# Optimization experiments

Hardware: AMD Instinct MI355X
Metric: run time of the kernel (lower is better)

Reference implementation:

```python
import jax
import jax.numpy as jnp
import numpy as np
from jax import lax

DELTA = float(np.exp(-2.0))  # rule-creation density threshold


def codebook_lamb(x):
    """Online growing RBF prototype codebook (ALMMo-style) for one layer.

    x: [N, M]. Returns lamb: [N] normalized density of each sample at its
    assigned rule. Faithful (corrected) semantics of Layer.__call__:
      - SEN = squared L2 norm per sample (over feature dim)
      - global mean / mean squared norm over the batch
      - sequential per-sample: if max RBF density over existing rules < exp(-2),
        append a new rule (prototype=c=x, SENc=||x||^2, support=1);
        else update rule_star. Note the source's `support[rule_star] = +1`
        assigns 1, so the running mean update degenerates to c[rule_star]=x,
        SENc[rule_star]=||x||^2 -- replicated here.
      - distances use the (never-updated) prototypes; bandwidth stau uses c.
    """
    N, M = x.shape
    SENx = jnp.sum(x * x, axis=-1)                      # [N]
    gmean = jnp.mean(x, axis=0)                         # [M]
    base = jnp.mean(SENx) - jnp.sum(gmean * gmean)      # SENgmean - SEN(gmean)
    R = N                                               # worst case: one rule/sample

    protos0 = jnp.zeros((R, M), x.dtype)
    pn20 = jnp.zeros((R,), x.dtype)                     # ||proto_r||^2 (carried)
    c0 = jnp.zeros((R, M), x.dtype)
    cn20 = jnp.zeros((R,), x.dtype)                     # ||c_r||^2 (carried)
    SENc0 = jnp.zeros((R,), x.dtype)
    count0 = jnp.int32(0)

    ridx = jnp.arange(R)

    def step(carry, inp):
        protos, pn2, c, cn2, SENc, count = carry
        xi, sxi = inp                                   # [M], scalar
        valid = ridx < count
        stau = (base + SENc - cn2) * 0.5                # [R]
        dist = sxi + pn2 - 2.0 * (protos @ xi)          # [R] ||xi - proto_r||^2
        dens = jnp.where(valid, jnp.exp(-dist / stau), -jnp.inf)
        idx = jnp.argmax(dens)
        vmax = dens[idx]
        new = (count == 0) | (vmax < DELTA)
        slot = jnp.where(new, count, idx)
        # both branches set c/SENc at slot to xi/sxi (support resets to 1)
        c = c.at[slot].set(xi)
        cn2 = cn2.at[slot].set(sxi)
        SENc = SENc.at[slot].set(sxi)
        # only a new rule writes a prototype (OOB scatter when count==R is dropped)
        protos = protos.at[count].set(jnp.where(new, xi, protos[count]))
        pn2 = pn2.at[count].set(jnp.where(new, sxi, pn2[count]))
        count = count + new.astype(count.dtype)
        return (protos, pn2, c, cn2, SENc, count), slot

    (protos, pn2, c, cn2, SENc, count), rules = lax.scan(
        step, (protos0, pn20, c0, cn20, SENc0, count0), (x, SENx)
    )

    # final densities of all samples under all (valid) rules: [R, N]
    stau = (base + SENc - cn2) * 0.5                    # [R]
    dist = SENx[None, :] + pn2[:, None] - 2.0 * (protos @ x.T)
    dens = jnp.where((ridx < count)[:, None], jnp.exp(-dist / stau[:, None]), 0.0)
    dens_xn = dens[rules, jnp.arange(N)]                # density at assigned rule
    lamb = dens_xn / jnp.sum(dens, axis=0)              # normalize over rules
    return lamb


def setup_inputs() -> dict:
    key = jax.random.key(0)
    k = jax.random.split(key, 5)
    N, D_IN, D_H, D_OUT = 2048, 2048, 2048, 1024
    s0 = 1.0 / np.sqrt(D_IN)
    s1 = 1.0 / np.sqrt(D_H)
    return {
        "x": jax.random.normal(k[0], (N, D_IN), jnp.float32),
        "W0": jax.random.normal(k[1], (D_H, D_IN), jnp.float32) * s0,
        "b0": jax.random.normal(k[2], (D_H,), jnp.float32) * s0,
        "W1": jax.random.normal(k[3], (D_OUT, D_H), jnp.float32) * s1,
        "b1": jax.random.normal(k[4], (D_OUT,), jnp.float32) * s1,
    }


def reference(x, W0, b0, W1, b1):
    lambs = []
    h = x
    for W, b in ((W0, b0), (W1, b1)):
        lambs.append(codebook_lamb(h))          # per-layer codebook on layer input
        h = jax.nn.sigmoid(h @ W.T + b)         # torch.nn.Linear + sigmoid
    return h, jnp.stack(lambs)                  # ([N, d_out], [n_layers, N])
```

## Files before the change

### kernel.cpp

```cpp
#include <hip/hip_runtime.h>
#include <cstdint>
#include <cstddef>


#define DELTA_F 0.13533528323661270f
#define MBYTE (1u << 20)

typedef __bf16 bf16;
typedef bf16 bf16x8 __attribute__((ext_vector_type(8)));
typedef bf16 bf16x4 __attribute__((ext_vector_type(4)));
typedef float f32x4 __attribute__((ext_vector_type(4)));

typedef __attribute__((address_space(1))) void as1_void;
typedef __attribute__((address_space(3))) void as3_void;

__device__ __forceinline__ void gload16(const bf16* g, bf16* l) {
  __builtin_amdgcn_global_load_lds((as1_void*)g, (as3_void*)l, 16, 0, 0);
}

template <bool SIG_B16>
__global__ __launch_bounds__(512, 4) void gemm_fused(
    const bf16* __restrict__ A, const bf16* __restrict__ Bm,
    float* __restrict__ G, bf16* __restrict__ Hb, float* __restrict__ Fo,
    const float* __restrict__ bias, float* __restrict__ SEN,
    float* __restrict__ sumAll, int K, int sigW) {
  __shared__ __align__(16) char smem[32768];
  const int tid = threadIdx.x;
  const int wave = tid >> 6, lane = tid & 63;
  const int quad = lane >> 4, l16 = lane & 15;
  const int kg = wave & 1, wm = (wave >> 1) & 1, wn = (wave >> 2) & 1;
  const int m0 = blockIdx.y * 128, n0 = blockIdx.x * 128;
  const int waveM = wm * 64, waveN = wn * 64;
  const bool isGram = (n0 < 2048);
  const int sr8 = lane >> 3, slot = lane & 7;
  const int gk = (slot ^ sr8) * 8;
  const bf16* aSrc = A + (size_t)(m0 + wave * 16 + sr8) * K + gk;
  const bf16* bSrc = Bm + (size_t)(n0 + wave * 16 + sr8) * K + gk;
  char* const aDst = smem + wave * 2048;
  char* const bDst = smem + 16384 + wave * 2048;
  const int swz = ((kg * 4 + quad) ^ (l16 & 7)) * 16;
  const int aOff = (waveM + l16) * 128 + swz;
  const int bOff = 16384 + (waveN + l16) * 128 + swz;

  f32x4 acc[4][4] = {};

  for (int k0 = 0; k0 < K; k0 += 64) {
    gload16(aSrc + k0, (bf16*)aDst);
    gload16(aSrc + 8 * (size_t)K + k0, (bf16*)(aDst + 1024));
    gload16(bSrc + k0, (bf16*)bDst);
    gload16(bSrc + 8 * (size_t)K + k0, (bf16*)(bDst + 1024));
    __syncthreads();
    bf16x8 af[4], bfr[4];
#pragma unroll
    for (int i = 0; i < 4; ++i) af[i] = *(const bf16x8*)(smem + aOff + i * 2048);
#pragma unroll
    for (int j = 0; j < 4; ++j) bfr[j] = *(const bf16x8*)(smem + bOff + j * 2048);
#pragma unroll
    for (int i = 0; i < 4; ++i)
#pragma unroll
      for (int j = 0; j < 4; ++j)
        acc[i][j] = __builtin_amdgcn_mfma_f32_16x16x32_bf16(af[i], bfr[j], acc[i][j], 0, 0, 0);
    __syncthreads();
  }

  float gsum = 0.f;
  char* const ex = smem + (wn * 2 + wm) * 8192;
#pragma unroll
  for (int round = 0; round < 2; ++round) {
    __syncthreads();
    if (kg == 1) {
#pragma unroll
      for (int ii = 0; ii < 2; ++ii)
#pragma unroll
        for (int j = 0; j < 4; ++j)
          *(f32x4*)(ex + (ii * 4 + j) * 1024 + lane * 16) = acc[round * 2 + ii][j];
    }
    __syncthreads();
    if (kg == 0) {
#pragma unroll
      for (int ii = 0; ii < 2; ++ii) {
        const int i = round * 2 + ii;
#pragma unroll
        for (int j = 0; j < 4; ++j) {
          f32x4 v = acc[i][j] + *(const f32x4*)(ex + (ii * 4 + j) * 1024 + lane * 16);
          const int col = n0 + waveN + j * 16 + l16;
          const float bv = isGram ? 0.f : bias[col - 2048];
#pragma unroll
          for (int r = 0; r < 4; ++r) {
            const int row = m0 + waveM + i * 16 + quad * 4 + r;
            if (isGram) {
              const float val = v[r];
              G[(size_t)row * 2048 + col] = val;
              gsum += val;
              if (row == col) SEN[row] = val;
            } else {
              const float hv = 1.0f / (1.0f + expf(-(v[r] + bv)));
              const int c2 = col - 2048;
              if (SIG_B16) Hb[(size_t)row * 2048 + c2] = (bf16)hv;
              else Fo[(size_t)row * sigW + c2] = hv;
            }
          }
        }
      }
    }
  }
  if (isGram && kg == 0) {
    for (int off = 32; off > 0; off >>= 1) gsum += __shfl_down(gsum, off, 64);
    if (lane == 0) atomicAdd(sumAll, gsum);
  }
}

__device__ __forceinline__ float block_reduce_sum(float s, float* ws4) {
  for (int off = 32; off > 0; off >>= 1) s += __shfl_down(s, off, 64);
  const int tid = threadIdx.x;
  if ((tid & 63) == 0) ws4[tid >> 6] = s;
  __syncthreads();
  return ws4[0] + ws4[1] + ws4[2] + ws4[3];
}

__global__ void f2b_all(const float* __restrict__ x, const float* __restrict__ W0,
                        const float* __restrict__ W1, bf16* __restrict__ xb,
                        bf16* __restrict__ wb0, bf16* __restrict__ wb1,
                        float* __restrict__ scal) {
  const int idx = (blockIdx.x * 256 + threadIdx.x) * 4;
  if (blockIdx.x == 0 && threadIdx.x < 16) scal[threadIdx.x] = 0.f;
  const float* src;
  bf16* dst;
  int off;
  if (idx < 4194304) { src = x; dst = xb; off = idx; }
  else if (idx < 8388608) { src = W0; dst = wb0; off = idx - 4194304; }
  else { src = W1; dst = wb1; off = idx - 8388608; }
  f32x4 v = *(const f32x4*)(src + off);
  bf16x4 o;
  o.x = (bf16)v.x; o.y = (bf16)v.y; o.z = (bf16)v.z; o.w = (bf16)v.w;
  *(bf16x4*)(dst + off) = o;
}

__global__ void stau_kernel(const float* __restrict__ SEN, float* __restrict__ base,
                            int Nsamp) {
  const int tid = threadIdx.x;
  float s = 0.f;
  for (int i = tid; i < Nsamp; i += 256) s += SEN[i];
  __shared__ float ws4[4];
  const float tot = block_reduce_sum(s, ws4);
  if (tid == 0) {
    const float invN = 1.0f / (float)Nsamp;
    const float stau = 0.5f * (tot * invN - base[2] * invN * invN);
    base[0] = stau;
    base[1] = -1.0f / stau;
  }
}

__global__ void edgesum_kernel(const float* __restrict__ G, const float* __restrict__ SEN,
                               const float* __restrict__ base, int N,
                               int* __restrict__ e, float* __restrict__ S) {
  const int i = blockIdx.x, tid = threadIdx.x;
  const float ninv = base[1];
  const float si = SEN[i];
  const float* gi = G + (size_t)i * N;
  __shared__ int sflag;
  if (tid == 0) sflag = 0;
  __syncthreads();
  float s = 0.f;
  int f = 0;
  for (int j = tid; j < N; j += 256) {
    const float dens = expf((si + SEN[j] - 2.0f * gi[j]) * ninv);
    s += dens;
    if (j < i && dens >= DELTA_F) f = 1;
  }
  if (f) atomicOr(&sflag, 1);
  __shared__ float ws4[4];
  const float tot = block_reduce_sum(s, ws4);
  __syncthreads();
  if (tid == 0) { e[i] = sflag; S[i] = tot; }
}

__global__ void decide_kernel(const int* __restrict__ e, const float* __restrict__ G,
                              const float* __restrict__ SEN, const float* __restrict__ base,
                              int N, int* __restrict__ newflag, int* __restrict__ assigned,
                              int* __restrict__ rcnt, int* __restrict__ rlist) {
  __shared__ int s_flag[2048];
  __shared__ short s_list[2048];
  __shared__ short s_re[2048];
  __shared__ int s_T, s_reN;
  __shared__ int scan[256];
  __shared__ float rbest[256];
  __shared__ int rbj[256];
  const int tid = threadIdx.x;
  const float ninv = base[1];
  const int per = N / 256;
  int cnt = 0;
  for (int k = 0; k < per; ++k) {
    const int i = tid * per + k;
    const int ei = e[i];
    s_flag[i] = (ei == 0);
    if (ei == 0) { newflag[i] = 1; assigned[i] = i; }
    cnt += ei;
  }
  scan[tid] = cnt;
  if (tid == 0) s_reN = 0;
  __syncthreads();
  for (int off = 1; off < 256; off <<= 1) {
    const int v = scan[tid];
    const int add = (tid >= off) ? scan[tid - off] : 0;
    __syncthreads();
    scan[tid] = v + add;
    __syncthreads();
  }
  int pos = scan[tid] - cnt;
  for (int k = 0; k < per; ++k) {
    const int i = tid * per + k;
    if (!s_flag[i]) s_list[pos++] = (short)i;
  }
  if (tid == 255) s_T = scan[255];
  __syncthreads();
  const int T = s_T;
  for (int t = 0; t < T; ++t) {
    const int i = s_list[t];
    const float si = SEN[i];
    const float* gi = G + (size_t)i * N;
    float best = -1.0f;
    int bestj = 0x7fffffff;
    for (int j = tid; j < i; j += 256) {
      if (s_flag[j]) {
        const float dens = expf((si + SEN[j] - 2.0f * gi[j]) * ninv);
        if (dens > best || (dens == best && j < bestj)) { best = dens; bestj = j; }
      }
    }
    rbest[tid] = best; rbj[tid] = bestj;
    __syncthreads();
    if (tid == 0) {
      float b = -1.0f;
      int bj = 0x7fffffff;
      for (int k = 0; k < 256; ++k)
        if (rbest[k] > b || (rbest[k] == b && rbj[k] < bj)) { b = rbest[k]; bj = rbj[k]; }
      if (b < DELTA_F) { s_flag[i] = 1; newflag[i] = 1; assigned[i] = i; }
      else { newflag[i] = 0; assigned[i] = bj; s_re[s_reN++] = (short)i; }
    }
    __syncthreads();
  }
  const int reN = s_reN;
  for (int t = tid; t < reN; t += 256) rlist[t] = s_re[t];
  if (tid == 0) rcnt[0] = reN;
}

__global__ void lamb_fix(const float* __restrict__ G, const float* __restrict__ SEN,
                         const float* __restrict__ base, const float* __restrict__ S,
                         const int* __restrict__ assigned, const int* __restrict__ rcnt,
                         const int* __restrict__ rlist, int N, float* __restrict__ lamb) {
  const int n = blockIdx.x * 256 + threadIdx.x;
  const float ninv = base[1];
  const float sn = SEN[n];
  const float* gn = G + (size_t)n * N;
  const int a = assigned[n];
  const float da = expf((sn + SEN[a] - 2.0f * gn[a]) * ninv);
  float denom = S[n];
  const int rc = rcnt[0];
  for (int t = 0; t < rc; ++t) {
    const int j = rlist[t];
    denom -= expf((sn + SEN[j] - 2.0f * gn[j]) * ninv);
  }
  lamb[n] = da / denom;
}

extern "C" void kernel_launch(void* const* d_in, const int* in_sizes, int n_in,
                              void* d_out, int out_size, void* d_ws, size_t ws_size,
                              hipStream_t stream) {
  const float* x = (const float*)d_in[0];
  const float* W0 = (const float*)d_in[1];
  const float* b0 = (const float*)d_in[2];
  const float* W1 = (const float*)d_in[3];
  const float* b1 = (const float*)d_in[4];
  float* out = (float*)d_out;

  const int N = 2048, DIN = 2048, DH = 2048, DOUT = 1024;

  char* w = (char*)d_ws;
  bf16* xb = (bf16*)(w);
  bf16* wb0 = (bf16*)(w + 8 * MBYTE);
  bf16* hb = (bf16*)(w + 16 * MBYTE);
  bf16* wb1 = (bf16*)(w + 24 * MBYTE);
  float* G = (float*)(w + 28 * MBYTE);
  float* SEN = (float*)(w + 44 * MBYTE);
  float* S = SEN + 2048;
  float* scal = S + 2048;
  int* e = (int*)(scal + 16);
  int* nf = e + 2048;
  int* as = nf + 2048;
  int* rcnt = as + 2048;
  int* rlist = rcnt + 16;

  float* lamb0 = out + (size_t)N * DOUT;
  float* lamb1 = lamb0 + N;

  f2b_all<<<10240, 256, 0, stream>>>(x, W0, W1, xb, wb0, wb1, scal);

  gemm_fused<true><<<dim3(32, 16), 512, 0, stream>>>(
      xb, xb, G, hb, nullptr, b0, SEN, scal + 2, DIN, DH);
  stau_kernel<<<1, 256, 0, stream>>>(SEN, scal + 0, N);
  edgesum_kernel<<<N, 256, 0, stream>>>(G, SEN, scal + 0, N, e, S);
  decide_kernel<<<1, 256, 0, stream>>>(e, G, SEN, scal + 0, N, nf, as, rcnt, rlist);
  lamb_fix<<<N / 256, 256, 0, stream>>>(G, SEN, scal + 0, S, as, rcnt, rlist, N, lamb0);

  gemm_fused<false><<<dim3(24, 16), 512, 0, stream>>>(
      hb, hb, G, nullptr, out, b1, SEN, scal + 6, DH, DOUT);
  stau_kernel<<<1, 256, 0, stream>>>(SEN, scal + 4, N);
  edgesum_kernel<<<N, 256, 0, stream>>>(G, SEN, scal + 4, N, e, S);
  decide_kernel<<<1, 256, 0, stream>>>(e, G, SEN, scal + 4, N, nf, as, rcnt, rlist);
  lamb_fix<<<N / 256, 256, 0, stream>>>(G, SEN, scal + 4, S, as, rcnt, rlist, N, lamb1);
}
```

Before: 231.6 us.

## Fuse density, row sums and edge flags into GEMM epilogue; precompute stau

The stau bandwidth is now computed before each Gram GEMM: for layer 0 from row norms and column sums produced during the bf16 conversion, and for layer 1 from norms and column sums accumulated in the layer-0 sigmoid epilogue. The GEMM epilogue can therefore write densities directly, accumulate per-row density sums and set the edge flags with atomics. This removes the separate edgesum pass over the Gram matrix and the recomputation of exp in the decide and lamb kernels. The lamb step is folded into the single-block decide kernel, which serializes that work onto one block, and the many extra atomics plus fast __expf bring some throughput and precision risk.

```diff
diff --git a/kernel.cpp b/kernel.cpp
--- a/kernel.cpp
+++ b/kernel.cpp
@@ -18,12 +18,14 @@
   __builtin_amdgcn_global_load_lds((as1_void*)g, (as3_void*)l, 16, 0, 0);
 }
 
-template <bool SIG_B16>
+template <bool IS_L0>
 __global__ __launch_bounds__(512, 4) void gemm_fused(
-    const bf16* __restrict__ A, const bf16* __restrict__ Bm,
-    float* __restrict__ G, bf16* __restrict__ Hb, float* __restrict__ Fo,
-    const float* __restrict__ bias, float* __restrict__ SEN,
-    float* __restrict__ sumAll, int K, int sigW) {
+    const bf16* __restrict__ A, float* __restrict__ Dens,
+    bf16* __restrict__ Hb, float* __restrict__ Fo,
+    const float* __restrict__ bias, const float* __restrict__ SENin,
+    const float* __restrict__ ninv_p, float* __restrict__ S,
+    int* __restrict__ e, float* __restrict__ SENhOut,
+    float* __restrict__ colsumH) {
   __shared__ __align__(16) char smem[32768];
   const int tid = threadIdx.x;
   const int wave = tid >> 6, lane = tid & 63;
@@ -34,8 +36,8 @@
   const bool isGram = (n0 < 2048);
   const int sr8 = lane >> 3, slot = lane & 7;
   const int gk = (slot ^ sr8) * 8;
-  const bf16* aSrc = A + (size_t)(m0 + wave * 16 + sr8) * K + gk;
-  const bf16* bSrc = Bm + (size_t)(n0 + wave * 16 + sr8) * K + gk;
+  const bf16* aSrc = A + (size_t)(m0 + wave * 16 + sr8) * 2048 + gk;
+  const bf16* bSrc = A + (size_t)(n0 + wave * 16 + sr8) * 2048 + gk;
   char* const aDst = smem + wave * 2048;
   char* const bDst = smem + 16384 + wave * 2048;
   const int swz = ((kg * 4 + quad) ^ (l16 & 7)) * 16;
@@ -43,12 +45,11 @@
   const int bOff = 16384 + (waveN + l16) * 128 + swz;
 
   f32x4 acc[4][4] = {};
-
-  for (int k0 = 0; k0 < K; k0 += 64) {
+  for (int k0 = 0; k0 < 2048; k0 += 64) {
     gload16(aSrc + k0, (bf16*)aDst);
-    gload16(aSrc + 8 * (size_t)K + k0, (bf16*)(aDst + 1024));
+    gload16(aSrc + 8 * 2048 + k0, (bf16*)(aDst + 1024));
     gload16(bSrc + k0, (bf16*)bDst);
-    gload16(bSrc + 8 * (size_t)K + k0, (bf16*)(bDst + 1024));
+    gload16(bSrc + 8 * 2048 + k0, (bf16*)(bDst + 1024));
     __syncthreads();
     bf16x8 af[4], bfr[4];
 #pragma unroll
@@ -63,7 +64,8 @@
     __syncthreads();
   }
 
-  float gsum = 0.f;
+  const float ninv = ninv_p[0];
+  float colp[4] = {0.f, 0.f, 0.f, 0.f};
   char* const ex = smem + (wn * 2 + wm) * 8192;
 #pragma unroll
   for (int round = 0; round < 2; ++round) {
@@ -80,151 +82,242 @@
 #pragma unroll
       for (int ii = 0; ii < 2; ++ii) {
         const int i = round * 2 + ii;
-#pragma unroll
-        for (int j = 0; j < 4; ++j) {
-          f32x4 v = acc[i][j] + *(const f32x4*)(ex + (ii * 4 + j) * 1024 + lane * 16);
-          const int col = n0 + waveN + j * 16 + l16;
-          const float bv = isGram ? 0.f : bias[col - 2048];
+        const int rbase = m0 + waveM + i * 16 + quad * 4;
+        if (isGram) {
+          const f32x4 si4 = *(const f32x4*)(SENin + rbase);
+          float rp[4] = {0.f, 0.f, 0.f, 0.f};
+          int er = 0;
+#pragma unroll
+          for (int j = 0; j < 4; ++j) {
+            f32x4 v = acc[i][j] + *(const f32x4*)(ex + (ii * 4 + j) * 1024 + lane * 16);
+            const int col = n0 + waveN + j * 16 + l16;
+            const float sj = SENin[col];
+#pragma unroll
+            for (int r = 0; r < 4; ++r) {
+              const float dens = __expf((si4[r] + sj - 2.0f * v[r]) * ninv);
+              Dens[(size_t)(rbase + r) * 2048 + col] = dens;
+              rp[r] += dens;
+              if (col < rbase + r && dens >= DELTA_F) er |= (1 << r);
+            }
+          }
 #pragma unroll
           for (int r = 0; r < 4; ++r) {
-            const int row = m0 + waveM + i * 16 + quad * 4 + r;
-            if (isGram) {
-              const float val = v[r];
-              G[(size_t)row * 2048 + col] = val;
-              gsum += val;
-              if (row == col) SEN[row] = val;
-            } else {
-              const float hv = 1.0f / (1.0f + expf(-(v[r] + bv)));
-              const int c2 = col - 2048;
-              if (SIG_B16) Hb[(size_t)row * 2048 + c2] = (bf16)hv;
-              else Fo[(size_t)row * sigW + c2] = hv;
+            float rv = rp[r];
+            rv += __shfl_xor(rv, 1, 64); rv += __shfl_xor(rv, 2, 64);
+            rv += __shfl_xor(rv, 4, 64); rv += __shfl_xor(rv, 8, 64);
+            if (l16 == 0) atomicAdd(S + rbase + r, rv);
+          }
+          er |= __shfl_xor(er, 1, 64); er |= __shfl_xor(er, 2, 64);
+          er |= __shfl_xor(er, 4, 64); er |= __shfl_xor(er, 8, 64);
+          if (l16 == 0 && er) {
+#pragma unroll
+            for (int r = 0; r < 4; ++r)
+              if ((er >> r) & 1) atomicOr(e + rbase + r, 1);
+          }
+        } else {
+          float rn[4] = {0.f, 0.f, 0.f, 0.f};
+#pragma unroll
+          for (int j = 0; j < 4; ++j) {
+            f32x4 v = acc[i][j] + *(const f32x4*)(ex + (ii * 4 + j) * 1024 + lane * 16);
+            const int c2 = n0 - 2048 + waveN + j * 16 + l16;
+            const float bv = bias[c2];
+#pragma unroll
+            for (int r = 0; r < 4; ++r) {
+              const float hv = 1.0f / (1.0f + __expf(-(v[r] + bv)));
+              if (IS_L0) {
+                Hb[(size_t)(rbase + r) * 2048 + c2] = (bf16)hv;
+                rn[r] += hv * hv;
+                colp[j] += hv;
+              } else {
+                Fo[(size_t)(rbase + r) * 1024 + c2] = hv;
+              }
+            }
+          }
+          if (IS_L0) {
+#pragma unroll
+            for (int r = 0; r < 4; ++r) {
+              float rv = rn[r];
+              rv += __shfl_xor(rv, 1, 64); rv += __shfl_xor(rv, 2, 64);
+              rv += __shfl_xor(rv, 4, 64); rv += __shfl_xor(rv, 8, 64);
+              if (l16 == 0) atomicAdd(SENhOut + rbase + r, rv);
             }
           }
         }
       }
     }
   }
-  if (isGram && kg == 0) {
-    for (int off = 32; off > 0; off >>= 1) gsum += __shfl_down(gsum, off, 64);
-    if (lane == 0) atomicAdd(sumAll, gsum);
-  }
-}
-
-__device__ __forceinline__ float block_reduce_sum(float s, float* ws4) {
-  for (int off = 32; off > 0; off >>= 1) s += __shfl_down(s, off, 64);
-  const int tid = threadIdx.x;
-  if ((tid & 63) == 0) ws4[tid >> 6] = s;
-  __syncthreads();
-  return ws4[0] + ws4[1] + ws4[2] + ws4[3];
+  if (IS_L0 && !isGram && kg == 0) {
+#pragma unroll
+    for (int j = 0; j < 4; ++j) {
+      float cv = colp[j];
+      cv += __shfl_xor(cv, 16, 64);
+      cv += __shfl_xor(cv, 32, 64);
+      if (lane < 16) atomicAdd(colsumH + (n0 - 2048 + waveN + j * 16 + lane), cv);
+    }
+  }
+}
+
+__device__ __forceinline__ float wave_reduce(float s) {
+  for (int o = 32; o > 0; o >>= 1) s += __shfl_down(s, o, 64);
+  return s;
 }
 
 __global__ void f2b_all(const float* __restrict__ x, const float* __restrict__ W0,
                         const float* __restrict__ W1, bf16* __restrict__ xb,
                         bf16* __restrict__ wb0, bf16* __restrict__ wb1,
-                        float* __restrict__ scal) {
-  const int idx = (blockIdx.x * 256 + threadIdx.x) * 4;
-  if (blockIdx.x == 0 && threadIdx.x < 16) scal[threadIdx.x] = 0.f;
-  const float* src;
-  bf16* dst;
-  int off;
-  if (idx < 4194304) { src = x; dst = xb; off = idx; }
-  else if (idx < 8388608) { src = W0; dst = wb0; off = idx - 4194304; }
-  else { src = W1; dst = wb1; off = idx - 8388608; }
-  f32x4 v = *(const f32x4*)(src + off);
-  bf16x4 o;
-  o.x = (bf16)v.x; o.y = (bf16)v.y; o.z = (bf16)v.z; o.w = (bf16)v.w;
-  *(bf16x4*)(dst + off) = o;
-}
-
-__global__ void stau_kernel(const float* __restrict__ SEN, float* __restrict__ base,
-                            int Nsamp) {
+                        float* __restrict__ SENx, float* __restrict__ cpartX) {
+  const int b = blockIdx.x, tid = threadIdx.x;
+  const int wave = tid >> 6, lane = tid & 63;
+  if (b < 256) {
+    const int r0 = b * 8;
+    __shared__ float ws[8][4];
+    f32x4 c0 = {0.f, 0.f, 0.f, 0.f}, c1 = {0.f, 0.f, 0.f, 0.f};
+    for (int r = 0; r < 8; ++r) {
+      const float* src = x + (size_t)(r0 + r) * 2048;
+      bf16* dst = xb + (size_t)(r0 + r) * 2048;
+      f32x4 v0 = *(const f32x4*)(src + tid * 4);
+      f32x4 v1 = *(const f32x4*)(src + 1024 + tid * 4);
+      bf16x4 o0, o1;
+      o0.x = (bf16)v0.x; o0.y = (bf16)v0.y; o0.z = (bf16)v0.z; o0.w = (bf16)v0.w;
+      o1.x = (bf16)v1.x; o1.y = (bf16)v1.y; o1.z = (bf16)v1.z; o1.w = (bf16)v1.w;
+      *(bf16x4*)(dst + tid * 4) = o0;
+      *(bf16x4*)(dst + 1024 + tid * 4) = o1;
+      c0 += v0; c1 += v1;
+      float rn = v0.x * v0.x + v0.y * v0.y + v0.z * v0.z + v0.w * v0.w +
+                 v1.x * v1.x + v1.y * v1.y + v1.z * v1.z + v1.w * v1.w;
+      rn = wave_reduce(rn);
+      if (lane == 0) ws[r][wave] = rn;
+    }
+    __syncthreads();
+    if (tid < 8) SENx[r0 + tid] = ws[tid][0] + ws[tid][1] + ws[tid][2] + ws[tid][3];
+    float* bin = cpartX + (size_t)(b & 15) * 2048;
+    atomicAdd(bin + tid * 4 + 0, c0.x); atomicAdd(bin + tid * 4 + 1, c0.y);
+    atomicAdd(bin + tid * 4 + 2, c0.z); atomicAdd(bin + tid * 4 + 3, c0.w);
+    atomicAdd(bin + 1024 + tid * 4 + 0, c1.x); atomicAdd(bin + 1024 + tid * 4 + 1, c1.y);
+    atomicAdd(bin + 1024 + tid * 4 + 2, c1.z); atomicAdd(bin + 1024 + tid * 4 + 3, c1.w);
+  } else if (b < 512) {
+    const size_t base = (size_t)(b - 256) * 16384;
+    for (int c = tid * 4; c < 16384; c += 1024) {
+      f32x4 v = *(const f32x4*)(W0 + base + c);
+      bf16x4 o;
+      o.x = (bf16)v.x; o.y = (bf16)v.y; o.z = (bf16)v.z; o.w = (bf16)v.w;
+      *(bf16x4*)(wb0 + base + c) = o;
+    }
+  } else {
+    const size_t base = (size_t)(b - 512) * 16384;
+    for (int c = tid * 4; c < 16384; c += 1024) {
+      f32x4 v = *(const f32x4*)(W1 + base + c);
+      bf16x4 o;
+      o.x = (bf16)v.x; o.y = (bf16)v.y; o.z = (bf16)v.z; o.w = (bf16)v.w;
+      *(bf16x4*)(wb1 + base + c) = o;
+    }
+  }
+}
+
+__global__ void stau0_kernel(const float* __restrict__ SENx,
+                             const float* __restrict__ cpartX,
+                             float* __restrict__ scal) {
   const int tid = threadIdx.x;
-  float s = 0.f;
-  for (int i = tid; i < Nsamp; i += 256) s += SEN[i];
-  __shared__ float ws4[4];
-  const float tot = block_reduce_sum(s, ws4);
+  float ssen = 0.f;
+  for (int i = tid; i < 2048; i += 256) ssen += SENx[i];
+  float sg2 = 0.f;
+  for (int c = tid; c < 2048; c += 256) {
+    float cs = 0.f;
+#pragma unroll
+    for (int p = 0; p < 16; ++p) cs += cpartX[(size_t)p * 2048 + c];
+    const float gm = cs * (1.f / 2048.f);
+    sg2 += gm * gm;
+  }
+  __shared__ float r1[256], r2[256];
+  r1[tid] = ssen; r2[tid] = sg2;
+  __syncthreads();
+  for (int s = 128; s; s >>= 1) {
+    if (tid < s) { r1[tid] += r1[tid + s]; r2[tid] += r2[tid + s]; }
+    __syncthreads();
+  }
   if (tid == 0) {
-    const float invN = 1.0f / (float)Nsamp;
-    const float stau = 0.5f * (tot * invN - base[2] * invN * invN);
-    base[0] = stau;
-    base[1] = -1.0f / stau;
-  }
-}
-
-__global__ void edgesum_kernel(const float* __restrict__ G, const float* __restrict__ SEN,
-                               const float* __restrict__ base, int N,
-                               int* __restrict__ e, float* __restrict__ S) {
-  const int i = blockIdx.x, tid = threadIdx.x;
-  const float ninv = base[1];
-  const float si = SEN[i];
-  const float* gi = G + (size_t)i * N;
-  __shared__ int sflag;
-  if (tid == 0) sflag = 0;
-  __syncthreads();
-  float s = 0.f;
-  int f = 0;
-  for (int j = tid; j < N; j += 256) {
-    const float dens = expf((si + SEN[j] - 2.0f * gi[j]) * ninv);
-    s += dens;
-    if (j < i && dens >= DELTA_F) f = 1;
-  }
-  if (f) atomicOr(&sflag, 1);
-  __shared__ float ws4[4];
-  const float tot = block_reduce_sum(s, ws4);
-  __syncthreads();
-  if (tid == 0) { e[i] = sflag; S[i] = tot; }
-}
-
-__global__ void decide_kernel(const int* __restrict__ e, const float* __restrict__ G,
-                              const float* __restrict__ SEN, const float* __restrict__ base,
-                              int N, int* __restrict__ newflag, int* __restrict__ assigned,
-                              int* __restrict__ rcnt, int* __restrict__ rlist) {
-  __shared__ int s_flag[2048];
+    const float stau = 0.5f * (r1[0] * (1.f / 2048.f) - r2[0]);
+    scal[0] = stau;
+    scal[1] = -1.f / stau;
+  }
+}
+
+template <bool STAU1>
+__global__ void decide_lamb(const int* __restrict__ e, const float* __restrict__ Dens,
+                            const float* __restrict__ S, float* __restrict__ lamb,
+                            const float* __restrict__ SENh,
+                            const float* __restrict__ colsumH,
+                            float* __restrict__ scalOut) {
+  __shared__ char s_flag[2048];
+  __shared__ short s_as[2048];
   __shared__ short s_list[2048];
   __shared__ short s_re[2048];
-  __shared__ int s_T, s_reN;
-  __shared__ int scan[256];
+  __shared__ int scan_[256];
   __shared__ float rbest[256];
   __shared__ int rbj[256];
+  __shared__ int s_T, s_reN;
+  __shared__ float r1[256], r2[256];
   const int tid = threadIdx.x;
-  const float ninv = base[1];
-  const int per = N / 256;
+
+  if (STAU1) {
+    float ssen = 0.f;
+    for (int i = tid; i < 2048; i += 256) ssen += SENh[i];
+    float sg2 = 0.f;
+    for (int c = tid; c < 2048; c += 256) {
+      const float gm = colsumH[c] * (1.f / 2048.f);
+      sg2 += gm * gm;
+    }
+    r1[tid] = ssen; r2[tid] = sg2;
+    __syncthreads();
+    for (int s = 128; s; s >>= 1) {
+      if (tid < s) { r1[tid] += r1[tid + s]; r2[tid] += r2[tid + s]; }
+      __syncthreads();
+    }
+    if (tid == 0) {
+      const float stau = 0.5f * (r1[0] * (1.f / 2048.f) - r2[0]);
+      scalOut[4] = stau;
+      scalOut[5] = -1.f / stau;
+    }
+    __syncthreads();
+  }
+
   int cnt = 0;
-  for (int k = 0; k < per; ++k) {
-    const int i = tid * per + k;
+#pragma unroll
+  for (int k = 0; k < 8; ++k) {
+    const int i = tid * 8 + k;
     const int ei = e[i];
     s_flag[i] = (ei == 0);
-    if (ei == 0) { newflag[i] = 1; assigned[i] = i; }
+    if (ei == 0) s_as[i] = (short)i;
     cnt += ei;
   }
-  scan[tid] = cnt;
+  scan_[tid] = cnt;
   if (tid == 0) s_reN = 0;
   __syncthreads();
   for (int off = 1; off < 256; off <<= 1) {
-    const int v = scan[tid];
-    const int add = (tid >= off) ? scan[tid - off] : 0;
-    __syncthreads();
-    scan[tid] = v + add;
-    __syncthreads();
-  }
-  int pos = scan[tid] - cnt;
-  for (int k = 0; k < per; ++k) {
-    const int i = tid * per + k;
+    const int v = scan_[tid];
+    const int add = (tid >= off) ? scan_[tid - off] : 0;
+    __syncthreads();
+    scan_[tid] = v + add;
+    __syncthreads();
+  }
+  int pos = scan_[tid] - cnt;
+#pragma unroll
+  for (int k = 0; k < 8; ++k) {
+    const int i = tid * 8 + k;
     if (!s_flag[i]) s_list[pos++] = (short)i;
   }
-  if (tid == 255) s_T = scan[255];
+  if (tid == 255) s_T = scan_[255];
   __syncthreads();
   const int T = s_T;
   for (int t = 0; t < T; ++t) {
     const int i = s_list[t];
-    const float si = SEN[i];
-    const float* gi = G + (size_t)i * N;
+    const float* di = Dens + (size_t)i * 2048;
     float best = -1.0f;
     int bestj = 0x7fffffff;
     for (int j = tid; j < i; j += 256) {
       if (s_flag[j]) {
-        const float dens = expf((si + SEN[j] - 2.0f * gi[j]) * ninv);
-        if (dens > best || (dens == best && j < bestj)) { best = dens; bestj = j; }
+        const float d = di[j];
+        if (d > best || (d == best && j < bestj)) { best = d; bestj = j; }
       }
     }
     rbest[tid] = best; rbj[tid] = bestj;
@@ -234,33 +327,19 @@
       int bj = 0x7fffffff;
       for (int k = 0; k < 256; ++k)
         if (rbest[k] > b || (rbest[k] == b && rbj[k] < bj)) { b = rbest[k]; bj = rbj[k]; }
-      if (b < DELTA_F) { s_flag[i] = 1; newflag[i] = 1; assigned[i] = i; }
-      else { newflag[i] = 0; assigned[i] = bj; s_re[s_reN++] = (short)i; }
+      if (b < DELTA_F) { s_flag[i] = 1; s_as[i] = (short)i; }
+      else { s_as[i] = (short)bj; s_re[s_reN++] = (short)i; }
     }
     __syncthreads();
   }
   const int reN = s_reN;
-  for (int t = tid; t < reN; t += 256) rlist[t] = s_re[t];
-  if (tid == 0) rcnt[0] = reN;
-}
-
-__global__ void lamb_fix(const float* __restrict__ G, const float* __restrict__ SEN,
-                         const float* __restrict__ base, const float* __restrict__ S,
-                         const int* __restrict__ assigned, const int* __restrict__ rcnt,
-                         const int* __restrict__ rlist, int N, float* __restrict__ lamb) {
-  const int n = blockIdx.x * 256 + threadIdx.x;
-  const float ninv = base[1];
-  const float sn = SEN[n];
-  const float* gn = G + (size_t)n * N;
-  const int a = assigned[n];
-  const float da = expf((sn + SEN[a] - 2.0f * gn[a]) * ninv);
-  float denom = S[n];
-  const int rc = rcnt[0];
-  for (int t = 0; t < rc; ++t) {
-    const int j = rlist[t];
-    denom -= expf((sn + SEN[j] - 2.0f * gn[j]) * ninv);
-  }
-  lamb[n] = da / denom;
+  for (int n = tid; n < 2048; n += 256) {
+    const int aa = s_as[n];
+    const float* dn = Dens + (size_t)n * 2048;
+    float denom = S[n];
+    for (int t = 0; t < reN; ++t) denom -= dn[s_re[t]];
+    lamb[n] = dn[aa] / denom;
+  }
 }
 
 extern "C" void kernel_launch(void* const* d_in, const int* in_sizes, int n_in,
@@ -273,39 +352,34 @@
   const float* b1 = (const float*)d_in[4];
   float* out = (float*)d_out;
 
-  const int N = 2048, DIN = 2048, DH = 2048, DOUT = 1024;
-
   char* w = (char*)d_ws;
   bf16* xb = (bf16*)(w);
   bf16* wb0 = (bf16*)(w + 8 * MBYTE);
   bf16* hb = (bf16*)(w + 16 * MBYTE);
   bf16* wb1 = (bf16*)(w + 24 * MBYTE);
-  float* G = (float*)(w + 28 * MBYTE);
-  float* SEN = (float*)(w + 44 * MBYTE);
-  float* S = SEN + 2048;
-  float* scal = S + 2048;
-  int* e = (int*)(scal + 16);
-  int* nf = e + 2048;
-  int* as = nf + 2048;
-  int* rcnt = as + 2048;
-  int* rlist = rcnt + 16;
-
-  float* lamb0 = out + (size_t)N * DOUT;
-  float* lamb1 = lamb0 + N;
-
-  f2b_all<<<10240, 256, 0, stream>>>(x, W0, W1, xb, wb0, wb1, scal);
-
+  float* Dens = (float*)(w + 28 * MBYTE);
+  float* SENx = (float*)(w + 44 * MBYTE);
+  float* scal = SENx + 2048;
+  float* zbase = scal + 16;
+  float* SENh = zbase;
+  float* cpartX = SENh + 2048;
+  float* colsumH = cpartX + 16 * 2048;
+  float* S0 = colsumH + 2048;
+  float* S1 = S0 + 2048;
+  int* e0 = (int*)(S1 + 2048);
+  int* e1 = e0 + 2048;
+  const size_t zbytes = (size_t)(2048 * 7 + 16 * 2048) * 4;
+
+  float* lamb0 = out + (size_t)2048 * 1024;
+  float* lamb1 = lamb0 + 2048;
+
+  hipMemsetAsync(zbase, 0, zbytes, stream);
+  f2b_all<<<640, 256, 0, stream>>>(x, W0, W1, xb, wb0, wb1, SENx, cpartX);
+  stau0_kernel<<<1, 256, 0, stream>>>(SENx, cpartX, scal);
   gemm_fused<true><<<dim3(32, 16), 512, 0, stream>>>(
-      xb, xb, G, hb, nullptr, b0, SEN, scal + 2, DIN, DH);
-  stau_kernel<<<1, 256, 0, stream>>>(SEN, scal + 0, N);
-  edgesum_kernel<<<N, 256, 0, stream>>>(G, SEN, scal + 0, N, e, S);
-  decide_kernel<<<1, 256, 0, stream>>>(e, G, SEN, scal + 0, N, nf, as, rcnt, rlist);
-  lamb_fix<<<N / 256, 256, 0, stream>>>(G, SEN, scal + 0, S, as, rcnt, rlist, N, lamb0);
-
+      xb, Dens, hb, nullptr, b0, SENx, scal + 1, S0, e0, SENh, colsumH);
+  decide_lamb<true><<<1, 256, 0, stream>>>(e0, Dens, S0, lamb0, SENh, colsumH, scal);
   gemm_fused<false><<<dim3(24, 16), 512, 0, stream>>>(
-      hb, hb, G, nullptr, out, b1, SEN, scal + 6, DH, DOUT);
-  stau_kernel<<<1, 256, 0, stream>>>(SEN, scal + 4, N);
-  edgesum_kernel<<<N, 256, 0, stream>>>(G, SEN, scal + 4, N, e, S);
-  decide_kernel<<<1, 256, 0, stream>>>(e, G, SEN, scal + 4, N, nf, as, rcnt, rlist);
-  lamb_fix<<<N / 256, 256, 0, stream>>>(G, SEN, scal + 4, S, as, rcnt, rlist, N, lamb1);
-}
+      hb, Dens, nullptr, out, b1, SENh, scal + 5, S1, e1, nullptr, nullptr);
+  decide_lamb<false><<<1, 256, 0, stream>>>(e1, Dens, S1, lamb1, nullptr, nullptr, nullptr);
+}
```

Result: faster. 207.5 us (-10.4%).
